# Optimization experiments

Hardware: AMD Instinct MI355X
Metric: run time of the kernel (lower is better)

## Reference

```python
import jax, jax.numpy as jnp
import numpy as np
from jax.scipy.special import logsumexp

B, N_LC, N_TE, D = 4, 2048, 2048, 256
ITERS = 100  # Sinkhorn iterations


def _mlp2(x, W1, b1, W2, b2):
    # 2-layer MLP with ReLU (DETR-style MLP, num_layers=2)
    h = jax.nn.relu(x @ W1.T + b1)
    return h @ W2.T + b2


def _log_optimal_transport(scores, alpha, iters):
    b, m, n = scores.shape
    ms = jnp.float32(m)
    ns = jnp.float32(n)
    # augment score matrix with dustbin row/col -> [b, m+1, n+1]
    bins0 = jnp.broadcast_to(alpha, (b, m, 1))
    bins1 = jnp.broadcast_to(alpha, (b, 1, n))
    binsc = jnp.broadcast_to(alpha, (b, 1, 1))
    Z = jnp.concatenate([
        jnp.concatenate([scores, bins0], axis=-1),
        jnp.concatenate([bins1, binsc], axis=-1)], axis=1)
    norm = -jnp.log(ms + ns)
    log_mu = jnp.concatenate([jnp.full((m,), norm), jnp.log(ns)[None] + norm])
    log_nu = jnp.concatenate([jnp.full((n,), norm), jnp.log(ms)[None] + norm])
    log_mu = jnp.broadcast_to(log_mu[None], (b, m + 1))
    log_nu = jnp.broadcast_to(log_nu[None], (b, n + 1))

    def step(carry, _):
        u, v = carry
        u = log_mu - logsumexp(Z + v[:, None, :], axis=2)
        v = log_nu - logsumexp(Z + u[:, :, None], axis=1)
        return (u, v), None

    u0 = jnp.zeros_like(log_mu)
    v0 = jnp.zeros_like(log_nu)
    (u, v), _ = jax.lax.scan(step, (u0, v0), None, length=iters)
    return Z + u[:, :, None] + v[:, None, :] - norm


def setup_inputs() -> dict:
    key = jax.random.key(0)
    ks = jax.random.split(key, 8)
    s = 1.0 / np.sqrt(D).astype(np.float32)
    return {
        "quer_feat_lc": jax.random.normal(ks[0], (B, N_LC, D), jnp.float32),
        "quer_feat_te": jax.random.normal(ks[1], (B, N_TE, D), jnp.float32),
        "W1_lc": jax.random.normal(ks[2], (D, D), jnp.float32) * s,
        "b1_lc": jnp.zeros((D,), jnp.float32),
        "W2_lc": jax.random.normal(ks[3], (D, D), jnp.float32) * s,
        "b2_lc": jnp.zeros((D,), jnp.float32),
        "W1_te": jax.random.normal(ks[4], (D, D), jnp.float32) * s,
        "b1_te": jnp.zeros((D,), jnp.float32),
        "W2_te": jax.random.normal(ks[5], (D, D), jnp.float32) * s,
        "b2_te": jnp.zeros((D,), jnp.float32),
        "bin_score": jnp.ones((), jnp.float32),
    }


def reference(quer_feat_lc, quer_feat_te, W1_lc, b1_lc, W2_lc, b2_lc,
              W1_te, b1_te, W2_te, b2_te, bin_score):
    f1 = _mlp2(quer_feat_lc, W1_lc, b1_lc, W2_lc, b2_lc)  # [B, N_LC, D]
    f2 = _mlp2(quer_feat_te, W1_te, b1_te, W2_te, b2_te)  # [B, N_TE, D]
    scores = jnp.einsum('bnc,bmc->bnm', f1, f2) / jnp.sqrt(jnp.float32(D))
    Z = _log_optimal_transport(scores, bin_score, ITERS)  # [B, N_LC+1, N_TE+1]
    return jnp.exp(Z)
```

## Files before the change

### kernel.cpp

```cpp
#include <hip/hip_runtime.h>
#include <hip/hip_fp16.h>

#define NQ   2048
#define NB   4
#define DD   256
#define M1   2049
#define STR  2064
#define SINK_ITERS 100
#define PNWG 256
#define PTPB 1024

typedef __attribute__((ext_vector_type(8))) short short8;
typedef __attribute__((ext_vector_type(4))) float floatx4;
typedef __attribute__((ext_vector_type(2))) float floatx2;

__device__ __forceinline__ unsigned short f2bf(float f) {
  unsigned u = __float_as_uint(f);
  u += 0x7FFF + ((u >> 16) & 1);
  return (unsigned short)(u >> 16);
}

__device__ __forceinline__ unsigned char f2fp8(float f) {
  unsigned short u = __half_as_ushort(__float2half(f));
  return (unsigned char)((u + 0x7F + ((u >> 8) & 1)) >> 8);
}

__device__ __forceinline__ int IDX(int j) { return j + (j >> 4); }

__global__ void k_cvt6(const float* __restrict__ x_lc, const float* __restrict__ x_te,
                       const float* __restrict__ w1lc, const float* __restrict__ w2lc,
                       const float* __restrict__ w1te, const float* __restrict__ w2te,
                       unsigned short* __restrict__ Xlc, unsigned short* __restrict__ Xte,
                       unsigned short* __restrict__ Wb) {
  const int NX4 = (NB * NQ * DD) / 4;
  const int NW4 = (DD * DD) / 4;
  int i4 = blockIdx.x * blockDim.x + threadIdx.x;
  const float* src; unsigned short* dst; int off;
  if (i4 < NX4)            { src = x_lc; dst = Xlc; off = i4; }
  else if (i4 < 2 * NX4)   { src = x_te; dst = Xte; off = i4 - NX4; }
  else {
    int k = i4 - 2 * NX4;
    int seg = k / NW4;
    off = k - seg * NW4;
    src = (seg == 0) ? w1lc : (seg == 1) ? w2lc : (seg == 2) ? w1te : w2te;
    dst = Wb + seg * 65536;
  }
  float4 f = ((const float4*)src)[off];
  ushort4 o;
  o.x = f2bf(f.x); o.y = f2bf(f.y); o.z = f2bf(f.z); o.w = f2bf(f.w);
  ((ushort4*)dst)[off] = o;
}

template<int MODE>
__global__ __launch_bounds__(256, 2)
void k_gemm_bt(const unsigned short* __restrict__ A,
               const unsigned short* __restrict__ Bt,
               void* __restrict__ Out, void* __restrict__ Out8,
               const float* __restrict__ bias, const float* __restrict__ bias2,
               int K, long aBatch, long bBatch, long oBatch, int ostride)
{
  __shared__ __align__(16) unsigned short lA[128 * 32];
  __shared__ __align__(16) unsigned short lB[128 * 32];
  const int tid  = threadIdx.x;
  const int lane = tid & 63;
  const int w    = tid >> 6;
  const int wm   = (w >> 1) * 64;
  const int wn   = (w & 1) * 64;
  const long bz  = blockIdx.z;
  const unsigned short* Ab = A  + bz * aBatch + (long)blockIdx.y * 128 * K;
  const unsigned short* Bb = Bt + bz * bBatch + (long)blockIdx.x * 128 * K;
  const float* bp = (bz == 0) ? bias : bias2;

  floatx4 acc[4][4];
  #pragma unroll
  for (int i = 0; i < 4; i++)
    #pragma unroll
    for (int j = 0; j < 4; j++) acc[i][j] = (floatx4){0.f, 0.f, 0.f, 0.f};

  for (int kt = 0; kt < K; kt += 32) {
    __syncthreads();
    #pragma unroll
    for (int s0 = 0; s0 < 512; s0 += 256) {
      int s = s0 + tid;
      int row = s >> 2, part = s & 3;
      ((uint4*)lA)[s] = *(const uint4*)(Ab + (long)row * K + kt + part * 8);
      ((uint4*)lB)[s] = *(const uint4*)(Bb + (long)row * K + kt + part * 8);
    }
    __syncthreads();
    const int kq = (lane >> 4) * 8;
    const int rl = lane & 15;
    short8 af[4], bf[4];
    #pragma unroll
    for (int t = 0; t < 4; t++) {
      af[t] = *(const short8*)(lA + (wm + t * 16 + rl) * 32 + kq);
      bf[t] = *(const short8*)(lB + (wn + t * 16 + rl) * 32 + kq);
    }
    #pragma unroll
    for (int i = 0; i < 4; i++)
      #pragma unroll
      for (int j = 0; j < 4; j++)
        acc[i][j] = __builtin_amdgcn_mfma_f32_16x16x32_bf16(af[i], bf[j], acc[i][j], 0, 0, 0);
  }

  const int cl = lane & 15, qd = lane >> 4;
  #pragma unroll
  for (int i = 0; i < 4; i++)
    #pragma unroll
    for (int j = 0; j < 4; j++) {
      const int col = blockIdx.x * 128 + wn + j * 16 + cl;
      const float bcol = (MODE >= 2) ? 0.f : bp[col];
      #pragma unroll
      for (int r = 0; r < 4; r++) {
        const long row = (long)blockIdx.y * 128 + wm + i * 16 + qd * 4 + r;
        float v = acc[i][j][r];
        if (MODE == 0) {
          v += bcol; v = v > 0.f ? v : 0.f;
          ((unsigned short*)Out)[bz * oBatch + row * ostride + col] = f2bf(v);
        } else if (MODE == 1) {
          v += bcol;
          ((unsigned short*)Out)[bz * oBatch + row * ostride + col] = f2bf(v);
        } else {
          v *= 0.0625f;
          v = fminf(fmaxf(v, -15.f), 10.9f);
          float e = __expf(v);
          const long idx = bz * oBatch + row * ostride + col;
          if (MODE == 2) ((__half*)Out)[idx] = __float2half(e);
          ((unsigned char*)Out8)[idx] = f2fp8(e);
        }
      }
    }
}

__global__ void k_fillinit(__half* __restrict__ E, const float* __restrict__ alphaPtr,
                           float* __restrict__ ev, unsigned* __restrict__ bar) {
  const float ea = __expf(*alphaPtr);
  const int idx = blockIdx.x * blockDim.x + threadIdx.x;
  const int n1 = NB * NQ * 16;
  if (idx < n1) {
    int b = idx / (NQ * 16);
    int rr = idx - b * NQ * 16;
    int i = rr >> 4;
    int j = 2048 + (rr & 15);
    E[((long)b * M1 + i) * STR + j] = (j == 2048) ? __float2half(ea) : __float2half(0.f);
  } else {
    int k = idx - n1;
    if (k < NB * STR) {
      int b = k / STR;
      int j = k - b * STR;
      E[((long)b * M1 + 2048) * STR + j] = (j <= 2048) ? __float2half(ea) : __float2half(0.f);
    }
  }
  if (idx < NB * STR) ev[idx] = 1.0f;
  if (idx < 2048) bar[idx] = 0u;
}

__device__ __forceinline__ void st_agent(float* p, float v) {
  __hip_atomic_store(p, v, __ATOMIC_RELAXED, __HIP_MEMORY_SCOPE_AGENT);
}
__device__ __forceinline__ float ld_agent(const float* p) {
  return __hip_atomic_load(p, __ATOMIC_RELAXED, __HIP_MEMORY_SCOPE_AGENT);
}
__device__ __forceinline__ unsigned ld_u32_agent(const unsigned* p) {
  return __hip_atomic_load(p, __ATOMIC_RELAXED, __HIP_MEMORY_SCOPE_AGENT);
}

__device__ __forceinline__ float wave_sum(float s) {
  #pragma unroll
  for (int o = 32; o; o >>= 1) s += __shfl_xor(s, o);
  return s;
}

__device__ __forceinline__ float dot16f8(uint4 hv, const float* wp) {
  const unsigned* u = (const unsigned*)&hv;
  float s = 0.f;
#if __has_builtin(__builtin_amdgcn_cvt_pk_f32_bf8)
  #pragma unroll
  for (int q = 0; q < 4; q++) {
    floatx2 lo = __builtin_amdgcn_cvt_pk_f32_bf8((int)u[q], false);
    floatx2 hi = __builtin_amdgcn_cvt_pk_f32_bf8((int)u[q], true);
    s += lo.x * wp[q * 4 + 0] + lo.y * wp[q * 4 + 1]
       + hi.x * wp[q * 4 + 2] + hi.y * wp[q * 4 + 3];
  }
#else
  const unsigned char* p = (const unsigned char*)&hv;
  #pragma unroll
  for (int t = 0; t < 16; t++) {
    unsigned short h = (unsigned short)p[t] << 8;
    s += __half2float(*reinterpret_cast<__half*>(&h)) * wp[t];
  }
#endif
  return s;
}

__global__ __launch_bounds__(PTPB, 4)
void k_sink(const unsigned char* __restrict__ E8, const unsigned char* __restrict__ ET8,
            float* __restrict__ eu, float* __restrict__ ev,
            const float* __restrict__ alphaPtr, unsigned* __restrict__ bar)
{
  __shared__ __align__(16) unsigned char rows[131072];
  __shared__ __align__(16) float sv[2200];
  const int tid  = threadIdx.x;
  const int wg   = blockIdx.x;
  const int b    = wg >> 6;
  const int g    = wg & 63;
  const int wv   = tid >> 6;
  const int lane = tid & 63;
  const int r0   = (g * 16 + wv) * 2;
  const float ea = __expf(alphaPtr[0]);
  const unsigned char* E8r  = E8  + ((long)b * M1 + r0) * STR;
  const unsigned char* ET8r = ET8 + ((long)b * M1 + r0) * STR;
  float* ub = eu + b * STR;
  float* vb = ev + b * STR;
  unsigned* cnt = bar + b * 64;
  unsigned* gen = bar + b * 64 + 32;
  const bool dustwave = (g == 63) && (wv == 15);

  {
    uint4* dw = (uint4*)(rows + wv * 8192);
    dw[lane]       = *(const uint4*)(E8r  +        lane * 16);
    dw[64 + lane]  = *(const uint4*)(E8r  + 1024 + lane * 16);
    dw[128 + lane] = *(const uint4*)(E8r  + STR  +        lane * 16);
    dw[192 + lane] = *(const uint4*)(E8r  + STR  + 1024 + lane * 16);
    dw[256 + lane] = *(const uint4*)(ET8r +        lane * 16);
    dw[320 + lane] = *(const uint4*)(ET8r + 1024 + lane * 16);
    dw[384 + lane] = *(const uint4*)(ET8r + STR  +        lane * 16);
    dw[448 + lane] = *(const uint4*)(ET8r + STR  + 1024 + lane * 16);
  }

  unsigned phase = 0;
  for (int it = 0; it < 2 * SINK_ITERS; ++it) {
    const float* vin = (it & 1) ? ub : vb;
    float*      vout = (it & 1) ? vb : ub;

    for (int j = tid; j < M1; j += PTPB) sv[IDX(j)] = ld_agent(vin + j);
    __syncthreads();

    const unsigned char* Rl = rows + wv * 8192 + ((it & 1) << 12);
    uint4 h0c0 = *(const uint4*)(Rl +        lane * 16);
    uint4 h0c1 = *(const uint4*)(Rl + 1024 + lane * 16);
    uint4 h1c0 = *(const uint4*)(Rl + 2048 + lane * 16);
    uint4 h1c1 = *(const uint4*)(Rl + 3072 + lane * 16);
    const float* w0 = sv + lane * 17;
    const float* w1 = sv + 1088 + lane * 17;
    float a0 = dot16f8(h0c0, w0) + dot16f8(h0c1, w1);
    float a1 = dot16f8(h1c0, w0) + dot16f8(h1c1, w1);
    a0 = wave_sum(a0);
    a1 = wave_sum(a1);
    if (lane == 0) {
      const float wd = ea * sv[IDX(2048)];
      st_agent(vout + r0,     (1.f / 4096.f) / (a0 + wd));
      st_agent(vout + r0 + 1, (1.f / 4096.f) / (a1 + wd));
    }

    if (dustwave) {
      float s = 0.f;
      #pragma unroll
      for (int t = 0; t < 16; t++) s += w0[t] + w1[t];
      s = wave_sum(s);
      if (lane == 0) st_agent(vout + 2048, 0.5f / (ea * (s + sv[IDX(2048)])));
    }

    ++phase;
    __syncthreads();
    if (tid == 0) {
      unsigned old = __hip_atomic_fetch_add(cnt, 1u, __ATOMIC_RELAXED, __HIP_MEMORY_SCOPE_AGENT);
      if (old == phase * 64u - 1u) {
        __hip_atomic_store(gen, phase, __ATOMIC_RELAXED, __HIP_MEMORY_SCOPE_AGENT);
      } else {
        while (ld_u32_agent(gen) < phase)
          __builtin_amdgcn_s_sleep(1);
      }
    }
    __syncthreads();
  }
}

__global__ void k_final(const __half* __restrict__ E, const float* __restrict__ eu,
                        const float* __restrict__ ev, float* __restrict__ out) {
  const int wv = blockIdx.x;
  const int b = wv / M1;
  const int i = wv - b * M1;
  const __half* R = E + ((long)b * M1 + i) * STR;
  const float ui = eu[b * STR + i] * 4096.f;
  const float* evb = ev + b * STR;
  float* orow = out + ((long)b * M1 + i) * M1;
  for (int j = threadIdx.x; j < M1; j += blockDim.x)
    orow[j] = __half2float(R[j]) * ui * evb[j];
}

extern "C" void kernel_launch(void* const* d_in, const int* in_sizes, int n_in,
                              void* d_out, int out_size, void* d_ws, size_t ws_size,
                              hipStream_t stream) {
  const float* x_lc  = (const float*)d_in[0];
  const float* x_te  = (const float*)d_in[1];
  const float* W1_lc = (const float*)d_in[2];
  const float* b1_lc = (const float*)d_in[3];
  const float* W2_lc = (const float*)d_in[4];
  const float* b2_lc = (const float*)d_in[5];
  const float* W1_te = (const float*)d_in[6];
  const float* b1_te = (const float*)d_in[7];
  const float* W2_te = (const float*)d_in[8];
  const float* b2_te = (const float*)d_in[9];
  const float* alpha = (const float*)d_in[10];

  char* ws = (char*)d_ws;
  unsigned short* Xlc = (unsigned short*)(ws + 0);
  unsigned short* Wb  = (unsigned short*)(ws + 8388608);
  unsigned short* H   = (unsigned short*)(ws + 8912896);
  unsigned short* F   = (unsigned short*)(ws + 0);
  __half* E  = (__half*)(ws + 21495808);
  unsigned char* E8  = (unsigned char*)(ws + 55328896);
  unsigned char* ET8 = (unsigned char*)(ws + 72245440);
  float* eu  = (float*)(ws + 89161984);
  float* ev  = (float*)(ws + 89195008);
  unsigned* bar = (unsigned*)(ws + 89228032);

  unsigned short* Xte = Xlc + 2097152;

  k_cvt6<<<4352, 256, 0, stream>>>(x_lc, x_te, W1_lc, W2_lc, W1_te, W2_te,
                                   Xlc, Xte, Wb);

  k_gemm_bt<0><<<dim3(2, 64, 2), 256, 0, stream>>>(Xlc, Wb,         H, nullptr, b1_lc, b1_te,
                                                   DD, 2097152, 131072, 2097152, DD);
  k_gemm_bt<1><<<dim3(2, 64, 2), 256, 0, stream>>>(H,   Wb + 65536, F, nullptr, b2_lc, b2_te,
                                                   DD, 2097152, 131072, 2097152, DD);

  unsigned short* F1 = F;
  unsigned short* F2 = F + 2097152;
  const long ab = (long)NQ * DD;
  const long ob = (long)M1 * STR;
  k_gemm_bt<2><<<dim3(16, 16, NB), 256, 0, stream>>>(F1, F2, E,  E8,  nullptr, nullptr, DD, ab, ab, ob, STR);
  k_gemm_bt<3><<<dim3(16, 16, NB), 256, 0, stream>>>(F2, F1, nullptr, ET8, nullptr, nullptr, DD, ab, ab, ob, STR);

  const int nfill = NB * NQ * 16 + NB * STR;
  k_fillinit<<<(nfill + 255) / 256, 256, 0, stream>>>(E, alpha, ev, bar);

  k_sink<<<PNWG, PTPB, 0, stream>>>(E8, ET8, eu, ev, alpha, bar);

  k_final<<<NB * M1, 256, 0, stream>>>(E, eu, ev, (float*)d_out);
}
```

Baseline: 878.1 us.

## Interleave two batches per Sinkhorn workgroup with split arrive/wait barriers

The persistent Sinkhorn kernel now has each workgroup own one row from each of two batches, using 128 workgroups per batch pair, instead of two rows of a single batch. Each half-iteration processes batch A and then batch B. The grid barrier is split so that a workgroup signals arrival for one batch and then works on the other batch before waiting. This hides the latency of the global spin barrier behind useful work. In exchange the kernel needs more barrier and syncthreads phases, a second shared vector buffer, and a different launch grid mapping that the host side must match.

```diff
diff --git a/kernel.cpp b/kernel.cpp
--- a/kernel.cpp
+++ b/kernel.cpp
@@ -198,77 +198,115 @@
             const float* __restrict__ alphaPtr, unsigned* __restrict__ bar)
 {
   __shared__ __align__(16) unsigned char rows[131072];
-  __shared__ __align__(16) float sv[2200];
+  __shared__ __align__(16) float svA[2200];
+  __shared__ __align__(16) float svB[2200];
   const int tid  = threadIdx.x;
   const int wg   = blockIdx.x;
-  const int b    = wg >> 6;
-  const int g    = wg & 63;
+  const int p    = wg >> 7;
+  const int g    = wg & 127;
   const int wv   = tid >> 6;
   const int lane = tid & 63;
-  const int r0   = (g * 16 + wv) * 2;
+  const int r    = g * 16 + wv;
   const float ea = __expf(alphaPtr[0]);
-  const unsigned char* E8r  = E8  + ((long)b * M1 + r0) * STR;
-  const unsigned char* ET8r = ET8 + ((long)b * M1 + r0) * STR;
-  float* ub = eu + b * STR;
-  float* vb = ev + b * STR;
-  unsigned* cnt = bar + b * 64;
-  unsigned* gen = bar + b * 64 + 32;
-  const bool dustwave = (g == 63) && (wv == 15);
+  const int bA = p * 2, bB = p * 2 + 1;
+  float* uA = eu + bA * STR;  float* vA = ev + bA * STR;
+  float* uB = eu + bB * STR;  float* vB = ev + bB * STR;
+  unsigned* cntA = bar + bA * 64;  unsigned* genA = cntA + 32;
+  unsigned* cntB = bar + bB * 64;  unsigned* genB = cntB + 32;
+  const bool dustw = (g == 127) && (wv == 15);
 
   {
     uint4* dw = (uint4*)(rows + wv * 8192);
-    dw[lane]       = *(const uint4*)(E8r  +        lane * 16);
-    dw[64 + lane]  = *(const uint4*)(E8r  + 1024 + lane * 16);
-    dw[128 + lane] = *(const uint4*)(E8r  + STR  +        lane * 16);
-    dw[192 + lane] = *(const uint4*)(E8r  + STR  + 1024 + lane * 16);
-    dw[256 + lane] = *(const uint4*)(ET8r +        lane * 16);
-    dw[320 + lane] = *(const uint4*)(ET8r + 1024 + lane * 16);
-    dw[384 + lane] = *(const uint4*)(ET8r + STR  +        lane * 16);
-    dw[448 + lane] = *(const uint4*)(ET8r + STR  + 1024 + lane * 16);
-  }
-
-  unsigned phase = 0;
-  for (int it = 0; it < 2 * SINK_ITERS; ++it) {
-    const float* vin = (it & 1) ? ub : vb;
-    float*      vout = (it & 1) ? vb : ub;
-
-    for (int j = tid; j < M1; j += PTPB) sv[IDX(j)] = ld_agent(vin + j);
-    __syncthreads();
-
-    const unsigned char* Rl = rows + wv * 8192 + ((it & 1) << 12);
-    uint4 h0c0 = *(const uint4*)(Rl +        lane * 16);
-    uint4 h0c1 = *(const uint4*)(Rl + 1024 + lane * 16);
-    uint4 h1c0 = *(const uint4*)(Rl + 2048 + lane * 16);
-    uint4 h1c1 = *(const uint4*)(Rl + 3072 + lane * 16);
-    const float* w0 = sv + lane * 17;
-    const float* w1 = sv + 1088 + lane * 17;
-    float a0 = dot16f8(h0c0, w0) + dot16f8(h0c1, w1);
-    float a1 = dot16f8(h1c0, w0) + dot16f8(h1c1, w1);
-    a0 = wave_sum(a0);
-    a1 = wave_sum(a1);
-    if (lane == 0) {
-      const float wd = ea * sv[IDX(2048)];
-      st_agent(vout + r0,     (1.f / 4096.f) / (a0 + wd));
-      st_agent(vout + r0 + 1, (1.f / 4096.f) / (a1 + wd));
-    }
-
-    if (dustwave) {
-      float s = 0.f;
-      #pragma unroll
-      for (int t = 0; t < 16; t++) s += w0[t] + w1[t];
-      s = wave_sum(s);
-      if (lane == 0) st_agent(vout + 2048, 0.5f / (ea * (s + sv[IDX(2048)])));
-    }
-
-    ++phase;
-    __syncthreads();
+    const unsigned char* pA  = E8  + ((long)bA * M1 + r) * STR;
+    const unsigned char* pAT = ET8 + ((long)bA * M1 + r) * STR;
+    const unsigned char* pB  = E8  + ((long)bB * M1 + r) * STR;
+    const unsigned char* pBT = ET8 + ((long)bB * M1 + r) * STR;
+    dw[lane]       = *(const uint4*)(pA  +        lane * 16);
+    dw[64 + lane]  = *(const uint4*)(pA  + 1024 + lane * 16);
+    dw[128 + lane] = *(const uint4*)(pAT +        lane * 16);
+    dw[192 + lane] = *(const uint4*)(pAT + 1024 + lane * 16);
+    dw[256 + lane] = *(const uint4*)(pB  +        lane * 16);
+    dw[320 + lane] = *(const uint4*)(pB  + 1024 + lane * 16);
+    dw[384 + lane] = *(const uint4*)(pBT +        lane * 16);
+    dw[448 + lane] = *(const uint4*)(pBT + 1024 + lane * 16);
+  }
+
+  const float* w0A = svA + lane * 17;
+  const float* w1A = svA + 1088 + lane * 17;
+  const float* w0B = svB + lane * 17;
+  const float* w1B = svB + 1088 + lane * 17;
+
+  for (int hp = 0; hp < 2 * SINK_ITERS; ++hp) {
+    const unsigned hpu = (unsigned)hp;
+    const float* vinA = (hp & 1) ? uA : vA;
+    float*      voutA = (hp & 1) ? vA : uA;
+    const float* vinB = (hp & 1) ? uB : vB;
+    float*      voutB = (hp & 1) ? vB : uB;
+
+    if (tid == 64 && hp > 0) {
+      unsigned old = __hip_atomic_fetch_add(cntB, 1u, __ATOMIC_RELAXED, __HIP_MEMORY_SCOPE_AGENT);
+      if (old == hpu * 128u - 1u)
+        __hip_atomic_store(genB, hpu, __ATOMIC_RELAXED, __HIP_MEMORY_SCOPE_AGENT);
+    }
     if (tid == 0) {
-      unsigned old = __hip_atomic_fetch_add(cnt, 1u, __ATOMIC_RELAXED, __HIP_MEMORY_SCOPE_AGENT);
-      if (old == phase * 64u - 1u) {
-        __hip_atomic_store(gen, phase, __ATOMIC_RELAXED, __HIP_MEMORY_SCOPE_AGENT);
-      } else {
-        while (ld_u32_agent(gen) < phase)
-          __builtin_amdgcn_s_sleep(1);
+      while (ld_u32_agent(genA) < hpu)
+        __builtin_amdgcn_s_sleep(1);
+    }
+    __syncthreads();
+
+    for (int j = tid; j < M1; j += PTPB) svA[IDX(j)] = ld_agent(vinA + j);
+    __syncthreads();
+
+    {
+      const unsigned char* R = rows + wv * 8192 + ((hp & 1) << 11);
+      uint4 c0 = *(const uint4*)(R +        lane * 16);
+      uint4 c1 = *(const uint4*)(R + 1024 + lane * 16);
+      float a = dot16f8(c0, w0A) + dot16f8(c1, w1A);
+      a = wave_sum(a);
+      if (lane == 0) {
+        const float wd = ea * svA[IDX(2048)];
+        st_agent(voutA + r, (1.f / 4096.f) / (a + wd));
+      }
+      if (dustw) {
+        float s = 0.f;
+        #pragma unroll
+        for (int t = 0; t < 16; t++) s += w0A[t] + w1A[t];
+        s = wave_sum(s);
+        if (lane == 0) st_agent(voutA + 2048, 0.5f / (ea * (s + svA[IDX(2048)])));
+      }
+    }
+    __syncthreads();
+
+    if (tid == 64) {
+      unsigned old = __hip_atomic_fetch_add(cntA, 1u, __ATOMIC_RELAXED, __HIP_MEMORY_SCOPE_AGENT);
+      if (old == (hpu + 1u) * 128u - 1u)
+        __hip_atomic_store(genA, hpu + 1u, __ATOMIC_RELAXED, __HIP_MEMORY_SCOPE_AGENT);
+    }
+    if (tid == 0) {
+      while (ld_u32_agent(genB) < hpu)
+        __builtin_amdgcn_s_sleep(1);
+    }
+    __syncthreads();
+
+    for (int j = tid; j < M1; j += PTPB) svB[IDX(j)] = ld_agent(vinB + j);
+    __syncthreads();
+
+    {
+      const unsigned char* R = rows + wv * 8192 + 4096 + ((hp & 1) << 11);
+      uint4 c0 = *(const uint4*)(R +        lane * 16);
+      uint4 c1 = *(const uint4*)(R + 1024 + lane * 16);
+      float a = dot16f8(c0, w0B) + dot16f8(c1, w1B);
+      a = wave_sum(a);
+      if (lane == 0) {
+        const float wd = ea * svB[IDX(2048)];
+        st_agent(voutB + r, (1.f / 4096.f) / (a + wd));
+      }
+      if (dustw) {
+        float s = 0.f;
+        #pragma unroll
+        for (int t = 0; t < 16; t++) s += w0B[t] + w1B[t];
+        s = wave_sum(s);
+        if (lane == 0) st_agent(voutB + 2048, 0.5f / (ea * (s + svB[IDX(2048)])));
       }
     }
     __syncthreads();
```

Result: slower. 1.033 ms (+17.7%).

## Use fp16 packed dot products for Sinkhorn matvec with rescaled scaling vectors

Applied to the files above, without the earlier changes.

Stores the Sinkhorn scaling vector in shared memory as packed fp16 pairs, rescaled by 4096 and with new normalisation constants so the values stay in fp16 range. The byte-to-half decode of the matrix entries becomes byte permutes, and the multiply-adds become v_dot2 fp16 instructions. This cuts ALU work, LDS footprint and vector load count, and each thread now loads 64 bits at once. The barrier also reads the generation counter before the atomic add so a late waiter can skip spinning. In exchange the weights carry fp16 precision and the fdot2 accumulation changes rounding.

```diff
diff --git a/kernel.cpp b/kernel.cpp
--- a/kernel.cpp
+++ b/kernel.cpp
@@ -13,6 +13,7 @@
 typedef __attribute__((ext_vector_type(8))) short short8;
 typedef __attribute__((ext_vector_type(4))) float floatx4;
 typedef __attribute__((ext_vector_type(2))) float floatx2;
+typedef _Float16 h2 __attribute__((ext_vector_type(2)));
 
 __device__ __forceinline__ unsigned short f2bf(float f) {
   unsigned u = __float_as_uint(f);
@@ -25,7 +26,9 @@
   return (unsigned char)((u + 0x7F + ((u >> 8) & 1)) >> 8);
 }
 
-__device__ __forceinline__ int IDX(int j) { return j + (j >> 4); }
+__device__ __forceinline__ h2 as_h2(unsigned x) {
+  union { unsigned u; h2 h; } c; c.u = x; return c.h;
+}
 
 __global__ void k_cvt6(const float* __restrict__ x_lc, const float* __restrict__ x_te,
                        const float* __restrict__ w1lc, const float* __restrict__ w2lc,
@@ -160,6 +163,9 @@
 __device__ __forceinline__ float ld_agent(const float* p) {
   return __hip_atomic_load(p, __ATOMIC_RELAXED, __HIP_MEMORY_SCOPE_AGENT);
 }
+__device__ __forceinline__ unsigned long long ld64_agent(const unsigned long long* p) {
+  return __hip_atomic_load(p, __ATOMIC_RELAXED, __HIP_MEMORY_SCOPE_AGENT);
+}
 __device__ __forceinline__ unsigned ld_u32_agent(const unsigned* p) {
   return __hip_atomic_load(p, __ATOMIC_RELAXED, __HIP_MEMORY_SCOPE_AGENT);
 }
@@ -170,23 +176,25 @@
   return s;
 }
 
-__device__ __forceinline__ float dot16f8(uint4 hv, const float* wp) {
+__device__ __forceinline__ float dot16e5(uint4 hv, const unsigned* wp, float s) {
   const unsigned* u = (const unsigned*)&hv;
-  float s = 0.f;
-#if __has_builtin(__builtin_amdgcn_cvt_pk_f32_bf8)
+#if __has_builtin(__builtin_amdgcn_fdot2) && __has_builtin(__builtin_amdgcn_perm)
   #pragma unroll
   for (int q = 0; q < 4; q++) {
-    floatx2 lo = __builtin_amdgcn_cvt_pk_f32_bf8((int)u[q], false);
-    floatx2 hi = __builtin_amdgcn_cvt_pk_f32_bf8((int)u[q], true);
-    s += lo.x * wp[q * 4 + 0] + lo.y * wp[q * 4 + 1]
-       + hi.x * wp[q * 4 + 2] + hi.y * wp[q * 4 + 3];
+    unsigned lo = __builtin_amdgcn_perm(u[q], 0u, 0x05000400u);
+    unsigned hi = __builtin_amdgcn_perm(u[q], 0u, 0x07000600u);
+    s = __builtin_amdgcn_fdot2(as_h2(lo), as_h2(wp[2 * q]),     s, false);
+    s = __builtin_amdgcn_fdot2(as_h2(hi), as_h2(wp[2 * q + 1]), s, false);
   }
 #else
   const unsigned char* p = (const unsigned char*)&hv;
   #pragma unroll
   for (int t = 0; t < 16; t++) {
-    unsigned short h = (unsigned short)p[t] << 8;
-    s += __half2float(*reinterpret_cast<__half*>(&h)) * wp[t];
+    unsigned short he = (unsigned short)p[t] << 8;
+    unsigned wdw = wp[t >> 1];
+    unsigned short hw = (t & 1) ? (unsigned short)(wdw >> 16) : (unsigned short)(wdw & 0xFFFF);
+    s += __half2float(*reinterpret_cast<__half*>(&he)) *
+         __half2float(*reinterpret_cast<__half*>(&hw));
   }
 #endif
   return s;
@@ -198,7 +206,8 @@
             const float* __restrict__ alphaPtr, unsigned* __restrict__ bar)
 {
   __shared__ __align__(16) unsigned char rows[131072];
-  __shared__ __align__(16) float sv[2200];
+  __shared__ __align__(16) unsigned svh[1160];
+  __shared__ float sdust;
   const int tid  = threadIdx.x;
   const int wg   = blockIdx.x;
   const int b    = wg >> 6;
@@ -214,6 +223,7 @@
   unsigned* cnt = bar + b * 64;
   unsigned* gen = bar + b * 64 + 32;
   const bool dustwave = (g == 63) && (wv == 15);
+  const int sslot = (tid >> 9) * 576 + (tid & 511) + ((tid & 511) >> 3);
 
   {
     uint4* dw = (uint4*)(rows + wv * 8192);
@@ -227,12 +237,24 @@
     dw[448 + lane] = *(const uint4*)(ET8r + STR  + 1024 + lane * 16);
   }
 
+  const unsigned* w0 = svh + 9 * lane;
+  const unsigned* w1 = svh + 576 + 9 * lane;
+  const unsigned ONES2 = 0x3C003C00u;
+
   unsigned phase = 0;
   for (int it = 0; it < 2 * SINK_ITERS; ++it) {
     const float* vin = (it & 1) ? ub : vb;
     float*      vout = (it & 1) ? vb : ub;
 
-    for (int j = tid; j < M1; j += PTPB) sv[IDX(j)] = ld_agent(vin + j);
+    {
+      unsigned long long w8 = ld64_agent((const unsigned long long*)(vin + 2 * tid));
+      float flo = __uint_as_float((unsigned)w8) * 4096.f;
+      float fhi = __uint_as_float((unsigned)(w8 >> 32)) * 4096.f;
+      unsigned pk = ((unsigned)__half_as_ushort(__float2half(fhi)) << 16)
+                  |  (unsigned)__half_as_ushort(__float2half(flo));
+      svh[sslot] = pk;
+      if (tid == 0) sdust = ld_agent(vin + 2048) * 4096.f;
+    }
     __syncthreads();
 
     const unsigned char* Rl = rows + wv * 8192 + ((it & 1) << 12);
@@ -240,35 +262,49 @@
     uint4 h0c1 = *(const uint4*)(Rl + 1024 + lane * 16);
     uint4 h1c0 = *(const uint4*)(Rl + 2048 + lane * 16);
     uint4 h1c1 = *(const uint4*)(Rl + 3072 + lane * 16);
-    const float* w0 = sv + lane * 17;
-    const float* w1 = sv + 1088 + lane * 17;
-    float a0 = dot16f8(h0c0, w0) + dot16f8(h0c1, w1);
-    float a1 = dot16f8(h1c0, w0) + dot16f8(h1c1, w1);
+    float a0 = dot16e5(h0c1, w1, dot16e5(h0c0, w0, 0.f));
+    float a1 = dot16e5(h1c1, w1, dot16e5(h1c0, w0, 0.f));
     a0 = wave_sum(a0);
     a1 = wave_sum(a1);
     if (lane == 0) {
-      const float wd = ea * sv[IDX(2048)];
-      st_agent(vout + r0,     (1.f / 4096.f) / (a0 + wd));
-      st_agent(vout + r0 + 1, (1.f / 4096.f) / (a1 + wd));
+      const float wd = ea * sdust;
+      st_agent(vout + r0,     1.f / (a0 + wd));
+      st_agent(vout + r0 + 1, 1.f / (a1 + wd));
     }
 
     if (dustwave) {
       float s = 0.f;
-      #pragma unroll
-      for (int t = 0; t < 16; t++) s += w0[t] + w1[t];
+#if __has_builtin(__builtin_amdgcn_fdot2)
+      #pragma unroll
+      for (int k = 0; k < 8; k++) s = __builtin_amdgcn_fdot2(as_h2(w0[k]), as_h2(ONES2), s, false);
+      #pragma unroll
+      for (int k = 0; k < 8; k++) s = __builtin_amdgcn_fdot2(as_h2(w1[k]), as_h2(ONES2), s, false);
+#else
+      #pragma unroll
+      for (int k = 0; k < 8; k++) {
+        unsigned a = w0[k], c = w1[k];
+        unsigned short x0 = (unsigned short)a, x1 = (unsigned short)(a >> 16);
+        unsigned short y0 = (unsigned short)c, y1 = (unsigned short)(c >> 16);
+        s += __half2float(*reinterpret_cast<__half*>(&x0)) + __half2float(*reinterpret_cast<__half*>(&x1))
+           + __half2float(*reinterpret_cast<__half*>(&y0)) + __half2float(*reinterpret_cast<__half*>(&y1));
+      }
+#endif
       s = wave_sum(s);
-      if (lane == 0) st_agent(vout + 2048, 0.5f / (ea * (s + sv[IDX(2048)])));
+      if (lane == 0) st_agent(vout + 2048, 2048.f / (ea * (s + sdust)));
     }
 
     ++phase;
     __syncthreads();
     if (tid == 0) {
+      unsigned gpre = ld_u32_agent(gen);
       unsigned old = __hip_atomic_fetch_add(cnt, 1u, __ATOMIC_RELAXED, __HIP_MEMORY_SCOPE_AGENT);
       if (old == phase * 64u - 1u) {
         __hip_atomic_store(gen, phase, __ATOMIC_RELAXED, __HIP_MEMORY_SCOPE_AGENT);
       } else {
-        while (ld_u32_agent(gen) < phase)
+        while (gpre < phase) {
           __builtin_amdgcn_s_sleep(1);
+          gpre = ld_u32_agent(gen);
+        }
       }
     }
     __syncthreads();
```

Measured after the change: 789.0 us. 10.1% less time.
